# Kernel optimization log

Hardware: AMD Instinct MI355X
Metric: run time of the kernel (lower is better)

## Reference

```python
import jax, jax.numpy as jnp
import numpy as np
import math

D_POLY = 2  # polynomial order d
N_NODES = 50000
IN_FEATS = 128
H_FEATS = 64
N_EDGES = 800000


def calc_thetas(d):
    # Beta-wavelet polynomial coefficients (ascending order), matching calculate_theta2
    thetas = []
    for i in range(d + 1):
        p = np.poly1d([1.0])
        for _ in range(i):
            p = p * np.poly1d([0.5, 0.0])      # (x/2)
        for _ in range(d - i):
            p = p * np.poly1d([-0.5, 1.0])     # (1 - x/2)
        beta = math.gamma(i + 1) * math.gamma(d + 1 - i) / math.gamma(d + 2)
        p = p / beta
        asc = p.coeffs[::-1]                   # ascending coefficients
        asc = np.concatenate([asc, np.zeros(d + 1 - len(asc))])
        thetas.append(asc.astype(np.float32))
    return thetas

THETAS = calc_thetas(D_POLY)


def setup_inputs() -> dict:
    key = jax.random.key(0)
    ks = jax.random.split(key, 7)
    features = jax.random.normal(ks[0], (N_NODES, IN_FEATS), dtype=jnp.float32)
    src = jax.random.randint(ks[1], (N_EDGES,), 0, N_NODES)
    dst = jax.random.randint(ks[2], (N_EDGES,), 0, N_NODES)
    s1 = 1.0 / math.sqrt(IN_FEATS)
    W1 = jax.random.uniform(ks[3], (H_FEATS, IN_FEATS), jnp.float32, -s1, s1)
    b1 = jnp.zeros((H_FEATS,), jnp.float32)
    s2 = 1.0 / math.sqrt(H_FEATS * (D_POLY + 1))
    W2 = jax.random.uniform(ks[4], (H_FEATS, H_FEATS * (D_POLY + 1)), jnp.float32, -s2, s2)
    b2 = jnp.zeros((H_FEATS,), jnp.float32)
    return {"features": features, "src": src, "dst": dst,
            "W1": W1, "b1": b1, "W2": W2, "b2": b2}


def reference(features, src, dst, W1, b1, W2, b2):
    N = features.shape[0]
    # linear1 + ReLU
    x = jax.nn.relu(features @ W1.T + b1)  # [N, H]
    # D^{-1/2} from in-degrees (clamped at 1)
    deg = jax.ops.segment_sum(jnp.ones_like(dst, dtype=x.dtype), dst, num_segments=N)
    D_invsqrt = jnp.clip(deg, 1.0, None) ** -0.5  # [N]
    D_invsqrt = D_invsqrt[:, None]

    def unn_laplacian(f):
        # f - D^{-1/2} A D^{-1/2} f   (aggregation onto destination nodes)
        agg = jax.ops.segment_sum((f * D_invsqrt)[src], dst, num_segments=N)
        return f - agg * D_invsqrt

    outs = []
    for theta in THETAS:
        f = x
        h = theta[0] * x
        for k in range(1, len(theta)):
            f = unn_laplacian(f)
            h = h + theta[k] * f
        outs.append(h)
    feats_final = jnp.concatenate(outs, axis=-1)  # [N, H*(d+1)]
    return feats_final @ W2.T + b2
```

## Files before the change

kernel.cpp:

```cpp
#include <hip/hip_runtime.h>

#define NN 50000
#define NE 800000
#define INF 128
#define HF 64
#define K2 192
#define MAXDEG 64

typedef __attribute__((ext_vector_type(8))) short short8;
typedef __attribute__((ext_vector_type(4))) float float4v;
typedef __attribute__((ext_vector_type(4))) unsigned short ushort4v;
typedef __attribute__((ext_vector_type(2))) unsigned int uint2v;

__device__ inline unsigned short f2bf(float x) {
    unsigned int u = __float_as_uint(x);
    u += 0x7FFFu + ((u >> 16) & 1u);
    return (unsigned short)(u >> 16);
}
__device__ inline float bf2f(unsigned short h) {
    return __uint_as_float(((unsigned int)h) << 16);
}
__device__ inline float bflo(unsigned int p) { return __uint_as_float(p << 16); }
__device__ inline float bfhi(unsigned int p) { return __uint_as_float(p & 0xFFFF0000u); }


__global__ __launch_bounds__(256) void fill_ell_part(const int* __restrict__ src,
                                                     const int* __restrict__ dst,
                                                     int* __restrict__ cnt,
                                                     unsigned short* __restrict__ ell) {
    int chunk = blockIdx.x >> 3;
    int p     = blockIdx.x & 7;
    int e = chunk * 256 + threadIdx.x;
    if (e >= NE) return;
    int d = dst[e];
    if (d / 6250 != p) return;
    int pos = atomicAdd(&cnt[d], 1);
    if (pos < MAXDEG) ell[d * MAXDEG + pos] = (unsigned short)src[e];
}

__global__ void dinv_kernel(int* __restrict__ cnt, float* __restrict__ dinv,
                            unsigned short* __restrict__ hb0,
                            unsigned short* __restrict__ hb1) {
    int i = blockIdx.x * blockDim.x + threadIdx.x;
    if (i < NN) {
        int c = cnt[i];
        if (c > MAXDEG) c = MAXDEG;
        cnt[i] = c;
        dinv[i] = rsqrtf((float)(c < 1 ? 1 : c));
    }
    if (i < HF) {
        hb0[(size_t)NN * HF + i] = 0;
        hb1[(size_t)NN * HF + i] = 0;
    }
}


__global__ void pack_b(const float* __restrict__ W1, const float* __restrict__ W2,
                       unsigned short* __restrict__ Bp1, unsigned short* __restrict__ Bp2) {
    int gid = blockIdx.x * 256 + threadIdx.x;
    if (gid >= 20480) return;
    if (gid < 8192) {
        int j  = gid & 7;
        int l  = (gid >> 3) & 63;
        int nt = (gid >> 9) & 3;
        int kc = gid >> 11;
        int n = nt * 16 + (l & 15);
        int k = kc * 32 + (l >> 4) * 8 + j;
        Bp1[gid] = f2bf(W1[n * INF + k]);
    } else {
        int g = gid - 8192;
        int j  = g & 7;
        int l  = (g >> 3) & 63;
        int nt = (g >> 9) & 3;
        int kc = g >> 11;
        int n = nt * 16 + (l & 15);
        int k = kc * 32 + (l >> 4) * 8 + j;
        const float* row = W2 + (size_t)n * K2;
        float v;
        if (k < 64) {
            v = 3.0f * row[k];
        } else if (k < 128) {
            int c = k - 64;
            v = -3.0f * row[c] + 3.0f * row[64 + c];
        } else {
            int c = k - 128;
            v = 0.75f * row[c] - 1.5f * row[64 + c] + 0.75f * row[128 + c];
        }
        Bp2[g] = f2bf(v);
    }
}


__global__ __launch_bounds__(256) void gemm1_mfma(const float* __restrict__ F,
                                                  const unsigned short* __restrict__ Bp,
                                                  const float* __restrict__ b1,
                                                  const float* __restrict__ dinv,
                                                  unsigned short* __restrict__ xb,
                                                  unsigned short* __restrict__ hb0) {
    int tid  = threadIdx.x;
    int lane = tid & 63;
    int wv   = tid >> 6;
    int m0   = blockIdx.x * 64 + wv * 16;
    if (m0 >= NN) return;
    int mrow = lane & 15;
    int q    = lane >> 4;

    float4v acc[4];
#pragma unroll
    for (int nt = 0; nt < 4; ++nt) acc[nt] = (float4v){0.f, 0.f, 0.f, 0.f};

    const float* arow = F + (size_t)(m0 + mrow) * INF + q * 8;
#pragma unroll
    for (int kc = 0; kc < INF / 32; ++kc) {
        const float* ap = arow + kc * 32;
        float4v a0 = *reinterpret_cast<const float4v*>(ap);
        float4v a1 = *reinterpret_cast<const float4v*>(ap + 4);
        short8 af;
        af[0] = (short)f2bf(a0[0]); af[1] = (short)f2bf(a0[1]);
        af[2] = (short)f2bf(a0[2]); af[3] = (short)f2bf(a0[3]);
        af[4] = (short)f2bf(a1[0]); af[5] = (short)f2bf(a1[1]);
        af[6] = (short)f2bf(a1[2]); af[7] = (short)f2bf(a1[3]);
#pragma unroll
        for (int nt = 0; nt < 4; ++nt) {
            short8 bf = *reinterpret_cast<const short8*>(Bp + (((kc * 4 + nt) * 64 + lane) << 3));
            acc[nt] = __builtin_amdgcn_mfma_f32_16x16x32_bf16(af, bf, acc[nt], 0, 0, 0);
        }
    }

    float dn[4];
#pragma unroll
    for (int r = 0; r < 4; ++r) dn[r] = dinv[m0 + q * 4 + r];

#pragma unroll
    for (int nt = 0; nt < 4; ++nt) {
        int n = nt * 16 + mrow;
        float bv = b1[n];
#pragma unroll
        for (int r = 0; r < 4; ++r) {
            int node = m0 + q * 4 + r;
            float v = acc[nt][r] + bv;
            v = v > 0.0f ? v : 0.0f;
            xb [(size_t)node * HF + n] = f2bf(v);
            hb0[(size_t)node * HF + n] = f2bf(v * dn[r]);
        }
    }
}


template <bool WRITE_H>
__global__ __launch_bounds__(256) void gather_quad(const unsigned short* __restrict__ ell,
                                                   const int* __restrict__ cnt,
                                                   const float* __restrict__ dinv,
                                                   const unsigned short* __restrict__ fin,
                                                   const unsigned short* __restrict__ hb,
                                                   unsigned short* __restrict__ fout,
                                                   unsigned short* __restrict__ hout) {
    int lane  = threadIdx.x & 63;
    int wv    = threadIdx.x >> 6;
    int which = lane >> 4;
    int jj    = lane & 15;
    int n = blockIdx.x * 16 + wv * 4 + which;
    int deg = cnt[n];

    ushort4v ids = *reinterpret_cast<const ushort4v*>(ell + (size_t)n * MAXDEG + jj * 4);
    int slot = jj * 4;
    int s0 = (slot + 0 < deg) ? (int)ids[0] : NN;
    int s1 = (slot + 1 < deg) ? (int)ids[1] : NN;
    int s2 = (slot + 2 < deg) ? (int)ids[2] : NN;
    int s3 = (slot + 3 < deg) ? (int)ids[3] : NN;

    int wmax = deg;
    wmax = max(wmax, __shfl_xor(wmax, 16));
    wmax = max(wmax, __shfl_xor(wmax, 32));

    const uint2v* hbd = (const uint2v*)hb;
    int base = which * 16;

    float a0=0,a1=0,a2=0,a3=0;
    float b0=0,b1=0,b2=0,b3=0;
    float c0=0,c1=0,c2=0,c3=0;
    float d0=0,d1=0,d2=0,d3=0;

    for (int k = 0; k < wmax; k += 4) {
        int o = base + (k >> 2);
        int t0 = __shfl(s0, o), t1 = __shfl(s1, o);
        int t2 = __shfl(s2, o), t3 = __shfl(s3, o);
        uint2v p0 = hbd[(size_t)t0 * 16 + jj];
        uint2v p1 = hbd[(size_t)t1 * 16 + jj];
        uint2v p2 = hbd[(size_t)t2 * 16 + jj];
        uint2v p3 = hbd[(size_t)t3 * 16 + jj];
        a0 += bflo(p0[0]); a1 += bfhi(p0[0]); a2 += bflo(p0[1]); a3 += bfhi(p0[1]);
        b0 += bflo(p1[0]); b1 += bfhi(p1[0]); b2 += bflo(p1[1]); b3 += bfhi(p1[1]);
        c0 += bflo(p2[0]); c1 += bfhi(p2[0]); c2 += bflo(p2[1]); c3 += bfhi(p2[1]);
        d0 += bflo(p3[0]); d1 += bfhi(p3[0]); d2 += bflo(p3[1]); d3 += bfhi(p3[1]);
    }
    float e0 = (a0 + b0) + (c0 + d0);
    float e1 = (a1 + b1) + (c1 + d1);
    float e2 = (a2 + b2) + (c2 + d2);
    float e3 = (a3 + b3) + (c3 + d3);
    float dn = dinv[n];

    uint2v xv = ((const uint2v*)fin)[(size_t)n * 16 + jj];
    float f0 = bflo(xv[0]) - e0 * dn;
    float f1 = bfhi(xv[0]) - e1 * dn;
    float f2 = bflo(xv[1]) - e2 * dn;
    float f3 = bfhi(xv[1]) - e3 * dn;
    uint2v ov;
    ov[0] = (unsigned int)f2bf(f0) | ((unsigned int)f2bf(f1) << 16);
    ov[1] = (unsigned int)f2bf(f2) | ((unsigned int)f2bf(f3) << 16);
    ((uint2v*)fout)[(size_t)n * 16 + jj] = ov;
    if (WRITE_H) {
        uint2v hv;
        hv[0] = (unsigned int)f2bf(f0 * dn) | ((unsigned int)f2bf(f1 * dn) << 16);
        hv[1] = (unsigned int)f2bf(f2 * dn) | ((unsigned int)f2bf(f3 * dn) << 16);
        ((uint2v*)hout)[(size_t)n * 16 + jj] = hv;
    }
}


__global__ __launch_bounds__(256) void gemm2_mfma(const unsigned short* __restrict__ xb,
                                                  const unsigned short* __restrict__ f1b,
                                                  const unsigned short* __restrict__ f2b,
                                                  const unsigned short* __restrict__ Bp,
                                                  const float* __restrict__ b2,
                                                  float* __restrict__ out) {
    int tid  = threadIdx.x;
    int lane = tid & 63;
    int wv   = tid >> 6;
    int m0   = blockIdx.x * 64 + wv * 16;
    if (m0 >= NN) return;
    int mrow = lane & 15;
    int q    = lane >> 4;

    float4v acc[4];
#pragma unroll
    for (int nt = 0; nt < 4; ++nt) acc[nt] = (float4v){0.f, 0.f, 0.f, 0.f};

    const unsigned short* ax = xb  + (size_t)(m0 + mrow) * HF + q * 8;
    const unsigned short* a1 = f1b + (size_t)(m0 + mrow) * HF + q * 8;
    const unsigned short* a2 = f2b + (size_t)(m0 + mrow) * HF + q * 8;

#pragma unroll
    for (int kc = 0; kc < 6; ++kc) {
        short8 af;
        if (kc < 2)      af = *reinterpret_cast<const short8*>(ax + kc * 32);
        else if (kc < 4) af = *reinterpret_cast<const short8*>(a1 + (kc - 2) * 32);
        else             af = *reinterpret_cast<const short8*>(a2 + (kc - 4) * 32);
#pragma unroll
        for (int nt = 0; nt < 4; ++nt) {
            short8 bf = *reinterpret_cast<const short8*>(Bp + (((kc * 4 + nt) * 64 + lane) << 3));
            acc[nt] = __builtin_amdgcn_mfma_f32_16x16x32_bf16(af, bf, acc[nt], 0, 0, 0);
        }
    }

#pragma unroll
    for (int nt = 0; nt < 4; ++nt) {
        int n = nt * 16 + mrow;
        float bv = b2[n];
#pragma unroll
        for (int r = 0; r < 4; ++r) {
            int node = m0 + q * 4 + r;
            out[(size_t)node * HF + n] = acc[nt][r] + bv;
        }
    }
}


extern "C" void kernel_launch(void* const* d_in, const int* in_sizes, int n_in,
                              void* d_out, int out_size, void* d_ws, size_t ws_size,
                              hipStream_t stream) {
    const float* features = (const float*)d_in[0];
    const int*   src      = (const int*)d_in[1];
    const int*   dst      = (const int*)d_in[2];
    const float* W1       = (const float*)d_in[3];
    const float* b1       = (const float*)d_in[4];
    const float* W2       = (const float*)d_in[5];
    const float* b2       = (const float*)d_in[6];
    float* out = (float*)d_out;

    unsigned short* xb  = (unsigned short*)d_ws;
    unsigned short* hb0 = xb  + (size_t)NN * HF;
    unsigned short* f1b = hb0 + (size_t)(NN + 1) * HF;
    unsigned short* hb1 = f1b + (size_t)NN * HF;
    unsigned short* f2b = hb1 + (size_t)(NN + 1) * HF;
    unsigned short* Bp1 = f2b + (size_t)NN * HF;
    unsigned short* Bp2 = Bp1 + 8192;
    unsigned short* ell = Bp2 + 12288;
    int*   cnt  = (int*)(ell + (size_t)NN * MAXDEG);
    float* dinv = (float*)(cnt + NN);

    hipMemsetAsync(cnt, 0, NN * sizeof(int), stream);

    fill_ell_part<<<((NE + 255) / 256) * 8, 256, 0, stream>>>(src, dst, cnt, ell);
    dinv_kernel<<<(NN + 255) / 256, 256, 0, stream>>>(cnt, dinv, hb0, hb1);

    pack_b<<<80, 256, 0, stream>>>(W1, W2, Bp1, Bp2);

    gemm1_mfma<<<(NN + 63) / 64, 256, 0, stream>>>(features, Bp1, b1, dinv, xb, hb0);

    gather_quad<true ><<<NN / 16, 256, 0, stream>>>(ell, cnt, dinv, xb,  hb0, f1b, hb1);
    gather_quad<false><<<NN / 16, 256, 0, stream>>>(ell, cnt, dinv, f1b, hb1, f2b, nullptr);

    gemm2_mfma<<<(NN + 63) / 64, 256, 0, stream>>>(xb, f1b, f2b, Bp2, b2, out);
}
```

Baseline: 172.8 us.

## Sort nodes by degree via histogram permutation to balance gather wavefronts

Builds a degree histogram in dinv_kernel, scans it, and fills a permutation that groups nodes by in-degree. The gather kernels then process nodes in that order, so the four nodes sharing a wavefront have similar degrees and the wave-level max-degree loop wastes fewer iterations. The cnt memset is folded into pack_b, which now runs first. This adds two small kernels and an indirect node lookup, and output writes are no longer sequential, which may hurt locality.

```diff
diff --git a/kernel.cpp b/kernel.cpp
--- a/kernel.cpp
+++ b/kernel.cpp
@@ -6,6 +6,7 @@
 #define HF 64
 #define K2 192
 #define MAXDEG 64
+#define NBINS 65
 
 typedef __attribute__((ext_vector_type(8))) short short8;
 typedef __attribute__((ext_vector_type(4))) float float4v;
@@ -16,9 +17,6 @@
     unsigned int u = __float_as_uint(x);
     u += 0x7FFFu + ((u >> 16) & 1u);
     return (unsigned short)(u >> 16);
-}
-__device__ inline float bf2f(unsigned short h) {
-    return __uint_as_float(((unsigned int)h) << 16);
 }
 __device__ inline float bflo(unsigned int p) { return __uint_as_float(p << 16); }
 __device__ inline float bfhi(unsigned int p) { return __uint_as_float(p & 0xFFFF0000u); }
@@ -38,26 +36,63 @@
     if (pos < MAXDEG) ell[d * MAXDEG + pos] = (unsigned short)src[e];
 }
 
-__global__ void dinv_kernel(int* __restrict__ cnt, float* __restrict__ dinv,
-                            unsigned short* __restrict__ hb0,
-                            unsigned short* __restrict__ hb1) {
-    int i = blockIdx.x * blockDim.x + threadIdx.x;
+__global__ __launch_bounds__(256) void dinv_kernel(int* __restrict__ cnt,
+                                                   float* __restrict__ dinv,
+                                                   int* __restrict__ hist,
+                                                   unsigned short* __restrict__ hb0,
+                                                   unsigned short* __restrict__ hb1) {
+    __shared__ int lh[NBINS];
+    int tid = threadIdx.x;
+    if (tid < NBINS) lh[tid] = 0;
+    __syncthreads();
+    int i = blockIdx.x * 256 + tid;
     if (i < NN) {
         int c = cnt[i];
         if (c > MAXDEG) c = MAXDEG;
         cnt[i] = c;
         dinv[i] = rsqrtf((float)(c < 1 ? 1 : c));
+        atomicAdd(&lh[c], 1);
     }
     if (i < HF) {
         hb0[(size_t)NN * HF + i] = 0;
         hb1[(size_t)NN * HF + i] = 0;
     }
+    __syncthreads();
+    if (tid < NBINS && lh[tid] > 0) atomicAdd(&hist[tid], lh[tid]);
+}
+
+__global__ __launch_bounds__(64) void scan_bins(const int* __restrict__ hist,
+                                                int* __restrict__ cursor) {
+    int t = threadIdx.x;
+    int v = hist[t];
+    int s = v;
+#pragma unroll
+    for (int off = 1; off < 64; off <<= 1) {
+        int u = __shfl_up(s, off);
+        if (t >= off) s += u;
+    }
+    cursor[t] = s - v;
+    if (t == 63) cursor[64] = s;
+}
+
+__global__ __launch_bounds__(256) void perm_fill(const int* __restrict__ cnt,
+                                                 int* __restrict__ cursor,
+                                                 int* __restrict__ perm) {
+    int i = blockIdx.x * 256 + threadIdx.x;
+    if (i >= NN) return;
+    int pos = atomicAdd(&cursor[cnt[i]], 1);
+    perm[pos] = i;
 }
 
 
 __global__ void pack_b(const float* __restrict__ W1, const float* __restrict__ W2,
-                       unsigned short* __restrict__ Bp1, unsigned short* __restrict__ Bp2) {
+                       unsigned short* __restrict__ Bp1, unsigned short* __restrict__ Bp2,
+                       int* __restrict__ cnt, int* __restrict__ hist) {
     int gid = blockIdx.x * 256 + threadIdx.x;
+    for (int z = gid; z < NN + NBINS; z += 20480) {
+        if (z < NN) cnt[z] = 0;
+        else        hist[z - NN] = 0;
+    }
     if (gid >= 20480) return;
     if (gid < 8192) {
         int j  = gid & 7;
@@ -148,7 +183,8 @@
 
 
 template <bool WRITE_H>
-__global__ __launch_bounds__(256) void gather_quad(const unsigned short* __restrict__ ell,
+__global__ __launch_bounds__(256) void gather_quad(const int* __restrict__ perm,
+                                                   const unsigned short* __restrict__ ell,
                                                    const int* __restrict__ cnt,
                                                    const float* __restrict__ dinv,
                                                    const unsigned short* __restrict__ fin,
@@ -159,7 +195,7 @@
     int wv    = threadIdx.x >> 6;
     int which = lane >> 4;
     int jj    = lane & 15;
-    int n = blockIdx.x * 16 + wv * 4 + which;
+    int n = perm[blockIdx.x * 16 + wv * 4 + which];
     int deg = cnt[n];
 
     ushort4v ids = *reinterpret_cast<const ushort4v*>(ell + (size_t)n * MAXDEG + jj * 4);
@@ -286,20 +322,25 @@
     unsigned short* Bp1 = f2b + (size_t)NN * HF;
     unsigned short* Bp2 = Bp1 + 8192;
     unsigned short* ell = Bp2 + 12288;
-    int*   cnt  = (int*)(ell + (size_t)NN * MAXDEG);
-    float* dinv = (float*)(cnt + NN);
-
-    hipMemsetAsync(cnt, 0, NN * sizeof(int), stream);
+    int*   cnt    = (int*)(ell + (size_t)NN * MAXDEG);
+    float* dinv   = (float*)(cnt + NN);
+    int*   hist   = (int*)(dinv + NN);
+    int*   cursor = hist + NBINS;
+    int*   perm   = cursor + NBINS;
+
+    pack_b<<<80, 256, 0, stream>>>(W1, W2, Bp1, Bp2, cnt, hist);
 
     fill_ell_part<<<((NE + 255) / 256) * 8, 256, 0, stream>>>(src, dst, cnt, ell);
-    dinv_kernel<<<(NN + 255) / 256, 256, 0, stream>>>(cnt, dinv, hb0, hb1);
-
-    pack_b<<<80, 256, 0, stream>>>(W1, W2, Bp1, Bp2);
+
+    dinv_kernel<<<(NN + 255) / 256, 256, 0, stream>>>(cnt, dinv, hist, hb0, hb1);
+
+    scan_bins<<<1, 64, 0, stream>>>(hist, cursor);
+    perm_fill<<<(NN + 255) / 256, 256, 0, stream>>>(cnt, cursor, perm);
 
     gemm1_mfma<<<(NN + 63) / 64, 256, 0, stream>>>(features, Bp1, b1, dinv, xb, hb0);
 
-    gather_quad<true ><<<NN / 16, 256, 0, stream>>>(ell, cnt, dinv, xb,  hb0, f1b, hb1);
-    gather_quad<false><<<NN / 16, 256, 0, stream>>>(ell, cnt, dinv, f1b, hb1, f2b, nullptr);
+    gather_quad<true ><<<NN / 16, 256, 0, stream>>>(perm, ell, cnt, dinv, xb,  hb0, f1b, hb1);
+    gather_quad<false><<<NN / 16, 256, 0, stream>>>(perm, ell, cnt, dinv, f1b, hb1, f2b, nullptr);
 
     gemm2_mfma<<<(NN + 63) / 64, 256, 0, stream>>>(xb, f1b, f2b, Bp2, b2, out);
 }
```

Result: slower. 311.2 us (+80.0%).
